# Optimization experiments

Hardware: AMD Instinct MI355X
Metric: run time of the kernel (lower is better)

The kernel has to match this reference:

```python
import jax, jax.numpy as jnp
import numpy as np

N_NODES = 100000
N_EDGES = 1600000
IN_FEATS = 128
HIDDEN = 128
NUM_CLASSES = 64


def setup_inputs() -> dict:
    key = jax.random.key(0)
    k1, k2, k3, k4, k5 = jax.random.split(key, 5)
    inputs = jax.random.normal(k1, (N_NODES, IN_FEATS), dtype=jnp.float32)
    src = jax.random.randint(k2, (N_EDGES,), 0, N_NODES, dtype=jnp.int32)
    dst = jax.random.randint(k3, (N_EDGES,), 0, N_NODES, dtype=jnp.int32)
    W1 = jax.random.normal(k4, (IN_FEATS, HIDDEN), dtype=jnp.float32) / np.sqrt(IN_FEATS)
    b1 = jnp.zeros((HIDDEN,), dtype=jnp.float32)
    W2 = jax.random.normal(k5, (HIDDEN, NUM_CLASSES), dtype=jnp.float32) / np.sqrt(HIDDEN)
    b2 = jnp.zeros((NUM_CLASSES,), dtype=jnp.float32)
    return {"inputs": inputs, "src": src, "dst": dst, "W1": W1, "b1": b1, "W2": W2, "b2": b2}


def _graph_conv(x, src, dst, W, b, n_nodes):
    # DGL GraphConv, norm='both': h = D_in^{-1/2} A D_out^{-1/2} x W + b
    ones = jnp.ones(src.shape[0], dtype=x.dtype)
    deg_out = jax.ops.segment_sum(ones, src, num_segments=n_nodes)
    deg_in = jax.ops.segment_sum(ones, dst, num_segments=n_nodes)
    norm_src = jax.lax.rsqrt(jnp.clip(deg_out, 1.0))  # [N]
    norm_dst = jax.lax.rsqrt(jnp.clip(deg_in, 1.0))   # [N]
    x = x * norm_src[:, None]
    msgs = x[src]                                      # [E, d] gather
    agg = jax.ops.segment_sum(msgs, dst, num_segments=n_nodes)  # [N, d] scatter-add
    agg = agg * norm_dst[:, None]
    return agg @ W + b


def reference(inputs, src, dst, W1, b1, W2, b2):
    n = inputs.shape[0]
    h = _graph_conv(inputs, src, dst, W1, b1, n)
    h = jax.nn.relu(h)
    h = _graph_conv(h, src, dst, W2, b2, n)
    return h
```

## Files before the change

kernel.cpp:

```cpp
#include <hip/hip_runtime.h>
#include <hip/hip_bf16.h>

#define N_FEATS_IN 128
#define BK_BITS 8
#define BK_SIZE 256
#define EPB 4096
#define MAXNB 512

typedef _Float16 h8 __attribute__((ext_vector_type(8)));
typedef float    f4v __attribute__((ext_vector_type(4)));
typedef float    f8v __attribute__((ext_vector_type(8)));

__device__ inline int wave_incl_scan(int v) {
    const int lane = threadIdx.x & 63;
    for (int off = 1; off < 64; off <<= 1) {
        int u = __shfl_up(v, off, 64);
        if (lane >= off) v += u;
    }
    return v;
}

__device__ inline int block_excl_scan(int s, int* ws, int* total) {
    const int lane = threadIdx.x & 63, wid = threadIdx.x >> 6;
    int inc = wave_incl_scan(s);
    if (lane == 63) ws[wid] = inc;
    __syncthreads();
    int woff = 0;
#pragma unroll
    for (int w = 0; w < 4; ++w) woff += (w < wid) ? ws[w] : 0;
    if (total) *total = ws[0] + ws[1] + ws[2] + ws[3];
    return woff + inc - s;
}

__global__ __launch_bounds__(256) void hist_kernel(
    const int* __restrict__ src, const int* __restrict__ dst,
    int* __restrict__ bh_d, int* __restrict__ bh_s, int E, int NB) {
    __shared__ int hd[MAXNB];
    __shared__ int hs[MAXNB];
    const int t = threadIdx.x;
    for (int i = t; i < NB; i += 256) { hd[i] = 0; hs[i] = 0; }
    __syncthreads();
    const int base = blockIdx.x * EPB;
    const int end = min(base + EPB, E);
    for (int e = base + t; e < end; e += 256) {
        atomicAdd(&hd[dst[e] >> BK_BITS], 1);
        atomicAdd(&hs[src[e] >> BK_BITS], 1);
    }
    __syncthreads();
    for (int i = t; i < NB; i += 256) {
        bh_d[(size_t)blockIdx.x * NB + i] = hd[i];
        bh_s[(size_t)blockIdx.x * NB + i] = hs[i];
    }
}

__global__ __launch_bounds__(256) void colsum2_kernel(
    const int* __restrict__ bh_d, const int* __restrict__ bh_s,
    int* __restrict__ tot_d, int* __restrict__ tot_s, int NBLK, int NB) {
    __shared__ int ws[8];
    const int b = blockIdx.x;
    const int t = threadIdx.x;
    const int lane = t & 63, wid = t >> 6;
    int sd = 0, ss = 0;
    for (int r = t; r < NBLK; r += 256) {
        sd += bh_d[(size_t)r * NB + b];
        ss += bh_s[(size_t)r * NB + b];
    }
    for (int off = 1; off < 64; off <<= 1) {
        sd += __shfl_down(sd, off, 64);
        ss += __shfl_down(ss, off, 64);
    }
    if (lane == 0) { ws[wid] = sd; ws[4 + wid] = ss; }
    __syncthreads();
    if (t == 0) tot_d[b] = ws[0] + ws[1] + ws[2] + ws[3];
    if (t == 1) tot_s[b] = ws[4] + ws[5] + ws[6] + ws[7];
}

__global__ __launch_bounds__(256) void bscan2_kernel(
    const int* __restrict__ tot_d, const int* __restrict__ tot_s,
    int* __restrict__ gb_d, int* __restrict__ gb_s,
    int* __restrict__ row_ptr, int NB, int N, int E) {
    __shared__ int ws[4];
    const int t = threadIdx.x;
    {
        const int a = (2 * t < NB) ? tot_d[2 * t] : 0;
        const int b = (2 * t + 1 < NB) ? tot_d[2 * t + 1] : 0;
        const int excl = block_excl_scan(a + b, ws, nullptr);
        if (2 * t < NB) gb_d[2 * t] = excl;
        if (2 * t + 1 < NB) gb_d[2 * t + 1] = excl + a;
    }
    __syncthreads();
    {
        const int a = (2 * t < NB) ? tot_s[2 * t] : 0;
        const int b = (2 * t + 1 < NB) ? tot_s[2 * t + 1] : 0;
        const int excl = block_excl_scan(a + b, ws, nullptr);
        if (2 * t < NB) gb_s[2 * t] = excl;
        if (2 * t + 1 < NB) gb_s[2 * t + 1] = excl + a;
    }
    if (t == 0) { gb_d[NB] = E; gb_s[NB] = E; row_ptr[N] = E; }
}

__global__ __launch_bounds__(256) void colscan2_kernel(
    int* __restrict__ bh_d, int* __restrict__ bh_s,
    const int* __restrict__ gb_d, const int* __restrict__ gb_s,
    int NBLK, int NB) {
    __shared__ int ws[4];
    const int b = blockIdx.x;
    const int t = threadIdx.x;
    const int r0 = 2 * t, r1 = 2 * t + 1;
    {
        const int a = (r0 < NBLK) ? bh_d[(size_t)r0 * NB + b] : 0;
        const int c = (r1 < NBLK) ? bh_d[(size_t)r1 * NB + b] : 0;
        const int excl = block_excl_scan(a + c, ws, nullptr);
        const int base = gb_d[b];
        if (r0 < NBLK) bh_d[(size_t)r0 * NB + b] = base + excl;
        if (r1 < NBLK) bh_d[(size_t)r1 * NB + b] = base + excl + a;
    }
    __syncthreads();
    {
        const int a = (r0 < NBLK) ? bh_s[(size_t)r0 * NB + b] : 0;
        const int c = (r1 < NBLK) ? bh_s[(size_t)r1 * NB + b] : 0;
        const int excl = block_excl_scan(a + c, ws, nullptr);
        const int base = gb_s[b];
        if (r0 < NBLK) bh_s[(size_t)r0 * NB + b] = base + excl;
        if (r1 < NBLK) bh_s[(size_t)r1 * NB + b] = base + excl + a;
    }
}

__global__ __launch_bounds__(256) void scatter2_kernel(
    const int* __restrict__ src, const int* __restrict__ dst,
    const int* __restrict__ bh_d, const int* __restrict__ bh_s,
    unsigned int* __restrict__ ebuf, unsigned char* __restrict__ sbuf,
    int E, int NB) {
    __shared__ int cd[MAXNB];
    __shared__ int cs[MAXNB];
    const int t = threadIdx.x;
    for (int i = t; i < NB; i += 256) {
        cd[i] = bh_d[(size_t)blockIdx.x * NB + i];
        cs[i] = bh_s[(size_t)blockIdx.x * NB + i];
    }
    __syncthreads();
    const int base = blockIdx.x * EPB;
    const int end = min(base + EPB, E);
    for (int e = base + t; e < end; e += 256) {
        const int d = dst[e];
        const int s = src[e];
        const int pd = atomicAdd(&cd[d >> BK_BITS], 1);
        ebuf[pd] = ((unsigned)s << 8) | (unsigned)(d & (BK_SIZE - 1));
        const int ps = atomicAdd(&cs[s >> BK_BITS], 1);
        sbuf[ps] = (unsigned char)(s & (BK_SIZE - 1));
    }
}

__global__ __launch_bounds__(256) void bucket_csr_kernel(
    const unsigned int* __restrict__ ebuf, const int* __restrict__ gb_d,
    int* __restrict__ row_ptr, float* __restrict__ norm_dst,
    int* __restrict__ edge_src, int N) {
    __shared__ int cnt[BK_SIZE];
    __shared__ int lro[BK_SIZE];
    __shared__ int ws[4];
    const int b = blockIdx.x;
    const int t = threadIdx.x;
    const int beg = gb_d[b], end = gb_d[b + 1];

    cnt[t] = 0;
    __syncthreads();
    for (int j = beg + t; j < end; j += 256)
        atomicAdd(&cnt[ebuf[j] & (BK_SIZE - 1)], 1);
    __syncthreads();

    const int v = cnt[t];
    const int excl = block_excl_scan(v, ws, nullptr);
    lro[t] = beg + excl;
    const int node = b * BK_SIZE + t;
    if (node < N) {
        row_ptr[node] = beg + excl;
        norm_dst[node] = rsqrtf(fmaxf((float)v, 1.0f));
    }
    __syncthreads();
    cnt[t] = 0;
    __syncthreads();

    for (int j = beg + t; j < end; j += 256) {
        const unsigned int ed = ebuf[j];
        const int dl = ed & (BK_SIZE - 1);
        const int p = atomicAdd(&cnt[dl], 1);
        edge_src[lro[dl] + p] = (int)(ed >> 8);
    }
}

__global__ __launch_bounds__(256) void count_src_kernel(
    const unsigned char* __restrict__ sbuf, const int* __restrict__ gb_s,
    float* __restrict__ norm_src, int N) {
    __shared__ int cnt[BK_SIZE];
    const int b = blockIdx.x;
    const int t = threadIdx.x;
    const int beg = gb_s[b], end = gb_s[b + 1];
    cnt[t] = 0;
    __syncthreads();
    for (int j = beg + t; j < end; j += 256)
        atomicAdd(&cnt[sbuf[j]], 1);
    __syncthreads();
    const int node = b * BK_SIZE + t;
    if (node < N)
        norm_src[node] = rsqrtf(fmaxf((float)cnt[t], 1.0f));
}

template <int OC, bool XHALF>
__global__ __launch_bounds__(256) void mfma_gemm_kernel(
    const void* __restrict__ Xv, const float* __restrict__ W,
    const float* __restrict__ scale, _Float16* __restrict__ Y, int n) {
    constexpr int K = 128;
    constexpr int NT = OC / 16;
    constexpr int RPB = 128;
    __shared__ _Float16 Wf[NT * 4 * 64 * 8];

    const int tid = threadIdx.x;
    for (int i = tid; i < K * OC; i += 256) {
        const int k = i / OC, c = i % OC;
        const int t = c >> 4, s = k >> 5, q = (k >> 3) & 3, j = k & 7;
        Wf[(((t * 4 + s) * 4 + q) * 16 + (c & 15)) * 8 + j] = (_Float16)W[i];
    }
    __syncthreads();

    const int lane = tid & 63;
    const int wv = tid >> 6;
    const int m = lane & 15, q = lane >> 4;

#pragma unroll
    for (int it = 0; it < RPB / 64; ++it) {
        const int rbase = blockIdx.x * RPB + it * 64 + wv * 16;
        const int lrow = min(rbase + m, n - 1);

        h8 a[4];
        if constexpr (XHALF) {
            const _Float16* X = (const _Float16*)Xv;
            const _Float16* p = &X[(size_t)lrow * K + q * 8];
#pragma unroll
            for (int s = 0; s < 4; ++s) a[s] = *(const h8*)(p + s * 32);
        } else {
            const float* X = (const float*)Xv;
            const float* p = &X[(size_t)lrow * K + q * 8];
#pragma unroll
            for (int s = 0; s < 4; ++s) {
                const float4 u0 = *(const float4*)(p + s * 32);
                const float4 u1 = *(const float4*)(p + s * 32 + 4);
                h8 v;
                v[0] = (_Float16)u0.x; v[1] = (_Float16)u0.y;
                v[2] = (_Float16)u0.z; v[3] = (_Float16)u0.w;
                v[4] = (_Float16)u1.x; v[5] = (_Float16)u1.y;
                v[6] = (_Float16)u1.z; v[7] = (_Float16)u1.w;
                a[s] = v;
            }
        }

        f4v acc[NT];
#pragma unroll
        for (int t = 0; t < NT; ++t) acc[t] = (f4v)0.0f;

#pragma unroll
        for (int s = 0; s < 4; ++s) {
#pragma unroll
            for (int t = 0; t < NT; ++t) {
                const h8 b = *(const h8*)&Wf[((t * 4 + s) * 64 + lane) * 8];
                acc[t] = __builtin_amdgcn_mfma_f32_16x16x32_f16(
                    a[s], b, acc[t], 0, 0, 0);
            }
        }

#pragma unroll
        for (int r = 0; r < 4; ++r) {
            const int orow = rbase + q * 4 + r;
            if (orow < n) {
                const float sc = scale[orow];
#pragma unroll
                for (int t = 0; t < NT; ++t)
                    Y[(size_t)orow * OC + t * 16 + m] =
                        (_Float16)(acc[t][r] * sc);
            }
        }
    }
}

template <int FEAT, bool RELU, bool OUT_HALF>
__global__ __launch_bounds__(256) void gather_agg_kernel(
    const _Float16* __restrict__ T, const int* __restrict__ row_ptr,
    const int* __restrict__ edge_src, const float* __restrict__ norm_dst,
    const float* __restrict__ bias, void* __restrict__ outv, int n) {
    constexpr int TPN = FEAT / 8;
    constexpr int NPB = 256 / TPN;
    const int node = blockIdx.x * NPB + threadIdx.x / TPN;
    const int f8 = threadIdx.x % TPN;
    if (node >= n) return;
    const int beg = row_ptr[node];
    const int end = row_ptr[node + 1];
    const h8* T8 = (const h8*)T;

    f8v acc = (f8v)0.0f;
    int j = beg;
    for (; j + 7 < end; j += 8) {
        int s[8];
#pragma unroll
        for (int u = 0; u < 8; ++u) s[u] = edge_src[j + u];
        h8 a[8];
#pragma unroll
        for (int u = 0; u < 8; ++u) a[u] = T8[(size_t)s[u] * TPN + f8];
#pragma unroll
        for (int u = 0; u < 8; ++u)
            acc += __builtin_convertvector(a[u], f8v);
    }
    for (; j + 3 < end; j += 4) {
        int s[4];
#pragma unroll
        for (int u = 0; u < 4; ++u) s[u] = edge_src[j + u];
        h8 a[4];
#pragma unroll
        for (int u = 0; u < 4; ++u) a[u] = T8[(size_t)s[u] * TPN + f8];
#pragma unroll
        for (int u = 0; u < 4; ++u)
            acc += __builtin_convertvector(a[u], f8v);
    }
    for (; j < end; ++j)
        acc += __builtin_convertvector(T8[(size_t)edge_src[j] * TPN + f8], f8v);

    const float nd = norm_dst[node];
    float r[8];
#pragma unroll
    for (int k = 0; k < 8; ++k) {
        r[k] = acc[k] * nd + bias[f8 * 8 + k];
        if constexpr (RELU) r[k] = fmaxf(r[k], 0.0f);
    }

    if constexpr (OUT_HALF) {
        _Float16* out = (_Float16*)outv;
        h8 o;
#pragma unroll
        for (int k = 0; k < 8; ++k) o[k] = (_Float16)r[k];
        *(h8*)&out[(size_t)node * FEAT + f8 * 8] = o;
    } else {
        float* out = (float*)outv;
        float4 o0 = make_float4(r[0], r[1], r[2], r[3]);
        float4 o1 = make_float4(r[4], r[5], r[6], r[7]);
        *(float4*)&out[(size_t)node * FEAT + f8 * 8] = o0;
        *(float4*)&out[(size_t)node * FEAT + f8 * 8 + 4] = o1;
    }
}

extern "C" void kernel_launch(void* const* d_in, const int* in_sizes, int n_in,
                              void* d_out, int out_size, void* d_ws, size_t ws_size,
                              hipStream_t stream) {
    const float* x   = (const float*)d_in[0];
    const int*   src = (const int*)d_in[1];
    const int*   dst = (const int*)d_in[2];
    const float* W1  = (const float*)d_in[3];
    const float* b1  = (const float*)d_in[4];
    const float* W2  = (const float*)d_in[5];
    const float* b2  = (const float*)d_in[6];
    float* out = (float*)d_out;

    const int N = in_sizes[0] / N_FEATS_IN;
    const int E = in_sizes[1];
    const int NB = (N + BK_SIZE - 1) / BK_SIZE;
    const int NBLK = (E + EPB - 1) / EPB;

    auto align4 = [](size_t w) { return (w + 3) & ~(size_t)3; };
    char* base = (char*)d_ws;
    size_t off = 0;
    auto take = [&](size_t words) {
        char* p = base + off * 4;
        off = align4(off + words);
        return p;
    };
    int*   tot_d    = (int*)take(NB);
    int*   tot_s    = (int*)take(NB);
    int*   gb_d     = (int*)take(NB + 1);
    int*   gb_s     = (int*)take(NB + 1);
    int*   bh_d     = (int*)take((size_t)NBLK * NB);
    int*   bh_s     = (int*)take((size_t)NBLK * NB);
    unsigned int*  ebuf = (unsigned int*)take(E);
    unsigned char* sbuf = (unsigned char*)take((E + 3) / 4);
    int*   row_ptr  = (int*)take(N + 1);
    int*   edge_src = (int*)take(E);
    float* norms    = (float*)take(2 * (size_t)N);
    _Float16* t1    = (_Float16*)take((size_t)N * 64);
    _Float16* h1    = (_Float16*)take((size_t)N * 64);
    _Float16* t2    = (_Float16*)take((size_t)N * 32);
    float* norm_src = norms;
    float* norm_dst = norms + N;

    hist_kernel<<<NBLK, 256, 0, stream>>>(src, dst, bh_d, bh_s, E, NB);
    colsum2_kernel<<<NB, 256, 0, stream>>>(bh_d, bh_s, tot_d, tot_s, NBLK, NB);
    bscan2_kernel<<<1, 256, 0, stream>>>(tot_d, tot_s, gb_d, gb_s, row_ptr,
                                         NB, N, E);
    colscan2_kernel<<<NB, 256, 0, stream>>>(bh_d, bh_s, gb_d, gb_s, NBLK, NB);
    scatter2_kernel<<<NBLK, 256, 0, stream>>>(src, dst, bh_d, bh_s, ebuf, sbuf,
                                              E, NB);
    bucket_csr_kernel<<<NB, 256, 0, stream>>>(ebuf, gb_d, row_ptr, norm_dst,
                                              edge_src, N);
    count_src_kernel<<<NB, 256, 0, stream>>>(sbuf, gb_s, norm_src, N);

    mfma_gemm_kernel<128, false><<<(N + 127) / 128, 256, 0, stream>>>(
        x, W1, norm_src, t1, N);
    gather_agg_kernel<128, true, true><<<(N + 15) / 16, 256, 0, stream>>>(
        t1, row_ptr, edge_src, norm_dst, b1, h1, N);

    mfma_gemm_kernel<64, true><<<(N + 127) / 128, 256, 0, stream>>>(
        h1, W2, norm_src, t2, N);
    gather_agg_kernel<64, false, false><<<(N + 31) / 32, 256, 0, stream>>>(
        t2, row_ptr, edge_src, norm_dst, b2, out, N);
}
```

Baseline: 343.1 us.

## Split gather-aggregate over feature chunks and use nontemporal index loads

Rewrites the neighbor gather-aggregate so each block handles only one of eight feature slices for a larger group of nodes, aiming to shrink the working set of gathered rows per pass for better cache reuse. Index and row-pointer reads plus output stores become nontemporal, and the 8-edge unrolled loop is removed. The trade-off is that the CSR indices are re-read once per chunk and each per-row access becomes narrower, which may hurt coalescing.

```diff
diff --git a/kernel.cpp b/kernel.cpp
--- a/kernel.cpp
+++ b/kernel.cpp
@@ -282,51 +282,49 @@
 }
 
 template <int FEAT, bool RELU, bool OUT_HALF>
-__global__ __launch_bounds__(256) void gather_agg_kernel(
+__global__ __launch_bounds__(256) void gather_chunk_kernel(
     const _Float16* __restrict__ T, const int* __restrict__ row_ptr,
     const int* __restrict__ edge_src, const float* __restrict__ norm_dst,
     const float* __restrict__ bias, void* __restrict__ outv, int n) {
-    constexpr int TPN = FEAT / 8;
+    constexpr int CF = FEAT / 8;
+    constexpr int TPN = CF / 8;
     constexpr int NPB = 256 / TPN;
-    const int node = blockIdx.x * NPB + threadIdx.x / TPN;
+    constexpr int VS = FEAT / 8;
+
+    const int chunk = blockIdx.x & 7;
+    const int grp = blockIdx.x >> 3;
+    const int node = grp * NPB + threadIdx.x / TPN;
     const int f8 = threadIdx.x % TPN;
     if (node >= n) return;
-    const int beg = row_ptr[node];
-    const int end = row_ptr[node + 1];
+    const int beg = __builtin_nontemporal_load(&row_ptr[node]);
+    const int end = __builtin_nontemporal_load(&row_ptr[node + 1]);
     const h8* T8 = (const h8*)T;
+    const int voff = chunk * TPN + f8;
 
     f8v acc = (f8v)0.0f;
     int j = beg;
-    for (; j + 7 < end; j += 8) {
-        int s[8];
-#pragma unroll
-        for (int u = 0; u < 8; ++u) s[u] = edge_src[j + u];
-        h8 a[8];
-#pragma unroll
-        for (int u = 0; u < 8; ++u) a[u] = T8[(size_t)s[u] * TPN + f8];
-#pragma unroll
-        for (int u = 0; u < 8; ++u)
-            acc += __builtin_convertvector(a[u], f8v);
-    }
     for (; j + 3 < end; j += 4) {
         int s[4];
 #pragma unroll
-        for (int u = 0; u < 4; ++u) s[u] = edge_src[j + u];
+        for (int u = 0; u < 4; ++u)
+            s[u] = __builtin_nontemporal_load(&edge_src[j + u]);
         h8 a[4];
 #pragma unroll
-        for (int u = 0; u < 4; ++u) a[u] = T8[(size_t)s[u] * TPN + f8];
+        for (int u = 0; u < 4; ++u) a[u] = T8[(size_t)s[u] * VS + voff];
 #pragma unroll
         for (int u = 0; u < 4; ++u)
             acc += __builtin_convertvector(a[u], f8v);
     }
-    for (; j < end; ++j)
-        acc += __builtin_convertvector(T8[(size_t)edge_src[j] * TPN + f8], f8v);
+    for (; j < end; ++j) {
+        const int s = __builtin_nontemporal_load(&edge_src[j]);
+        acc += __builtin_convertvector(T8[(size_t)s * VS + voff], f8v);
+    }
 
     const float nd = norm_dst[node];
     float r[8];
 #pragma unroll
     for (int k = 0; k < 8; ++k) {
-        r[k] = acc[k] * nd + bias[f8 * 8 + k];
+        r[k] = acc[k] * nd + bias[chunk * CF + f8 * 8 + k];
         if constexpr (RELU) r[k] = fmaxf(r[k], 0.0f);
     }
 
@@ -335,13 +333,15 @@
         h8 o;
 #pragma unroll
         for (int k = 0; k < 8; ++k) o[k] = (_Float16)r[k];
-        *(h8*)&out[(size_t)node * FEAT + f8 * 8] = o;
+        __builtin_nontemporal_store(
+            o, (h8*)&out[(size_t)node * FEAT + chunk * CF + f8 * 8]);
     } else {
         float* out = (float*)outv;
-        float4 o0 = make_float4(r[0], r[1], r[2], r[3]);
-        float4 o1 = make_float4(r[4], r[5], r[6], r[7]);
-        *(float4*)&out[(size_t)node * FEAT + f8 * 8] = o0;
-        *(float4*)&out[(size_t)node * FEAT + f8 * 8 + 4] = o1;
+        f4v o0 = {r[0], r[1], r[2], r[3]};
+        f4v o1 = {r[4], r[5], r[6], r[7]};
+        float* p = &out[(size_t)node * FEAT + chunk * CF + f8 * 8];
+        __builtin_nontemporal_store(o0, (f4v*)p);
+        __builtin_nontemporal_store(o1, (f4v*)(p + 4));
     }
 }
 
@@ -400,11 +400,13 @@
 
     mfma_gemm_kernel<128, false><<<(N + 127) / 128, 256, 0, stream>>>(
         x, W1, norm_src, t1, N);
-    gather_agg_kernel<128, true, true><<<(N + 15) / 16, 256, 0, stream>>>(
+    gather_chunk_kernel<128, true, true>
+        <<<8 * ((N + 127) / 128), 256, 0, stream>>>(
         t1, row_ptr, edge_src, norm_dst, b1, h1, N);
 
     mfma_gemm_kernel<64, true><<<(N + 127) / 128, 256, 0, stream>>>(
         h1, W2, norm_src, t2, N);
-    gather_agg_kernel<64, false, false><<<(N + 31) / 32, 256, 0, stream>>>(
+    gather_chunk_kernel<64, false, false>
+        <<<8 * ((N + 255) / 256), 256, 0, stream>>>(
         t2, row_ptr, edge_src, norm_dst, b2, out, N);
 }
```

Result: slower. 778.3 us (+126.8%).

## Merge column sum and column scan, fold source-degree count into CSR kernel

Applied to the files above, without the earlier changes.

Replaces the separate column-sum and column-scan passes over the per-block histograms with a single kernel that computes local column prefixes and totals in one pass. The global bucket offsets are now added while the scatter kernel loads its counters. The source-degree counting kernel is folded into the bucket CSR kernel. Together this removes two kernel launches and one read/write pass over the histogram arrays, in exchange for a slightly longer serial tail in the fused CSR kernel.

```diff
diff --git a/kernel.cpp b/kernel.cpp
--- a/kernel.cpp
+++ b/kernel.cpp
@@ -53,26 +53,34 @@
     }
 }
 
-__global__ __launch_bounds__(256) void colsum2_kernel(
-    const int* __restrict__ bh_d, const int* __restrict__ bh_s,
+__global__ __launch_bounds__(256) void colprefix2_kernel(
+    int* __restrict__ bh_d, int* __restrict__ bh_s,
     int* __restrict__ tot_d, int* __restrict__ tot_s, int NBLK, int NB) {
-    __shared__ int ws[8];
+    __shared__ int ws[4];
     const int b = blockIdx.x;
     const int t = threadIdx.x;
-    const int lane = t & 63, wid = t >> 6;
-    int sd = 0, ss = 0;
-    for (int r = t; r < NBLK; r += 256) {
-        sd += bh_d[(size_t)r * NB + b];
-        ss += bh_s[(size_t)r * NB + b];
-    }
-    for (int off = 1; off < 64; off <<= 1) {
-        sd += __shfl_down(sd, off, 64);
-        ss += __shfl_down(ss, off, 64);
-    }
-    if (lane == 0) { ws[wid] = sd; ws[4 + wid] = ss; }
-    __syncthreads();
-    if (t == 0) tot_d[b] = ws[0] + ws[1] + ws[2] + ws[3];
-    if (t == 1) tot_s[b] = ws[4] + ws[5] + ws[6] + ws[7];
+    int carry = 0;
+    for (int base = 0; base < NBLK; base += 256) {
+        const int r = base + t;
+        const int v = (r < NBLK) ? bh_d[(size_t)r * NB + b] : 0;
+        int total;
+        const int e = block_excl_scan(v, ws, &total);
+        if (r < NBLK) bh_d[(size_t)r * NB + b] = carry + e;
+        carry += total;
+        __syncthreads();
+    }
+    if (t == 0) tot_d[b] = carry;
+    carry = 0;
+    for (int base = 0; base < NBLK; base += 256) {
+        const int r = base + t;
+        const int v = (r < NBLK) ? bh_s[(size_t)r * NB + b] : 0;
+        int total;
+        const int e = block_excl_scan(v, ws, &total);
+        if (r < NBLK) bh_s[(size_t)r * NB + b] = carry + e;
+        carry += total;
+        __syncthreads();
+    }
+    if (t == 0) tot_s[b] = carry;
 }
 
 __global__ __launch_bounds__(256) void bscan2_kernel(
@@ -99,44 +107,18 @@
     if (t == 0) { gb_d[NB] = E; gb_s[NB] = E; row_ptr[N] = E; }
 }
 
-__global__ __launch_bounds__(256) void colscan2_kernel(
-    int* __restrict__ bh_d, int* __restrict__ bh_s,
-    const int* __restrict__ gb_d, const int* __restrict__ gb_s,
-    int NBLK, int NB) {
-    __shared__ int ws[4];
-    const int b = blockIdx.x;
-    const int t = threadIdx.x;
-    const int r0 = 2 * t, r1 = 2 * t + 1;
-    {
-        const int a = (r0 < NBLK) ? bh_d[(size_t)r0 * NB + b] : 0;
-        const int c = (r1 < NBLK) ? bh_d[(size_t)r1 * NB + b] : 0;
-        const int excl = block_excl_scan(a + c, ws, nullptr);
-        const int base = gb_d[b];
-        if (r0 < NBLK) bh_d[(size_t)r0 * NB + b] = base + excl;
-        if (r1 < NBLK) bh_d[(size_t)r1 * NB + b] = base + excl + a;
-    }
-    __syncthreads();
-    {
-        const int a = (r0 < NBLK) ? bh_s[(size_t)r0 * NB + b] : 0;
-        const int c = (r1 < NBLK) ? bh_s[(size_t)r1 * NB + b] : 0;
-        const int excl = block_excl_scan(a + c, ws, nullptr);
-        const int base = gb_s[b];
-        if (r0 < NBLK) bh_s[(size_t)r0 * NB + b] = base + excl;
-        if (r1 < NBLK) bh_s[(size_t)r1 * NB + b] = base + excl + a;
-    }
-}
-
 __global__ __launch_bounds__(256) void scatter2_kernel(
     const int* __restrict__ src, const int* __restrict__ dst,
     const int* __restrict__ bh_d, const int* __restrict__ bh_s,
+    const int* __restrict__ gb_d, const int* __restrict__ gb_s,
     unsigned int* __restrict__ ebuf, unsigned char* __restrict__ sbuf,
     int E, int NB) {
     __shared__ int cd[MAXNB];
     __shared__ int cs[MAXNB];
     const int t = threadIdx.x;
     for (int i = t; i < NB; i += 256) {
-        cd[i] = bh_d[(size_t)blockIdx.x * NB + i];
-        cs[i] = bh_s[(size_t)blockIdx.x * NB + i];
+        cd[i] = bh_d[(size_t)blockIdx.x * NB + i] + gb_d[i];
+        cs[i] = bh_s[(size_t)blockIdx.x * NB + i] + gb_s[i];
     }
     __syncthreads();
     const int base = blockIdx.x * EPB;
@@ -153,14 +135,16 @@
 
 __global__ __launch_bounds__(256) void bucket_csr_kernel(
     const unsigned int* __restrict__ ebuf, const int* __restrict__ gb_d,
+    const unsigned char* __restrict__ sbuf, const int* __restrict__ gb_s,
     int* __restrict__ row_ptr, float* __restrict__ norm_dst,
-    int* __restrict__ edge_src, int N) {
+    float* __restrict__ norm_src, int* __restrict__ edge_src, int N) {
     __shared__ int cnt[BK_SIZE];
     __shared__ int lro[BK_SIZE];
     __shared__ int ws[4];
     const int b = blockIdx.x;
     const int t = threadIdx.x;
     const int beg = gb_d[b], end = gb_d[b + 1];
+    const int node = b * BK_SIZE + t;
 
     cnt[t] = 0;
     __syncthreads();
@@ -171,7 +155,6 @@
     const int v = cnt[t];
     const int excl = block_excl_scan(v, ws, nullptr);
     lro[t] = beg + excl;
-    const int node = b * BK_SIZE + t;
     if (node < N) {
         row_ptr[node] = beg + excl;
         norm_dst[node] = rsqrtf(fmaxf((float)v, 1.0f));
@@ -186,21 +169,14 @@
         const int p = atomicAdd(&cnt[dl], 1);
         edge_src[lro[dl] + p] = (int)(ed >> 8);
     }
-}
-
-__global__ __launch_bounds__(256) void count_src_kernel(
-    const unsigned char* __restrict__ sbuf, const int* __restrict__ gb_s,
-    float* __restrict__ norm_src, int N) {
-    __shared__ int cnt[BK_SIZE];
-    const int b = blockIdx.x;
-    const int t = threadIdx.x;
-    const int beg = gb_s[b], end = gb_s[b + 1];
+
+    __syncthreads();
     cnt[t] = 0;
     __syncthreads();
-    for (int j = beg + t; j < end; j += 256)
+    const int sb = gb_s[b], se = gb_s[b + 1];
+    for (int j = sb + t; j < se; j += 256)
         atomicAdd(&cnt[sbuf[j]], 1);
     __syncthreads();
-    const int node = b * BK_SIZE + t;
     if (node < N)
         norm_src[node] = rsqrtf(fmaxf((float)cnt[t], 1.0f));
 }
@@ -388,15 +364,14 @@
     float* norm_dst = norms + N;
 
     hist_kernel<<<NBLK, 256, 0, stream>>>(src, dst, bh_d, bh_s, E, NB);
-    colsum2_kernel<<<NB, 256, 0, stream>>>(bh_d, bh_s, tot_d, tot_s, NBLK, NB);
+    colprefix2_kernel<<<NB, 256, 0, stream>>>(bh_d, bh_s, tot_d, tot_s,
+                                              NBLK, NB);
     bscan2_kernel<<<1, 256, 0, stream>>>(tot_d, tot_s, gb_d, gb_s, row_ptr,
                                          NB, N, E);
-    colscan2_kernel<<<NB, 256, 0, stream>>>(bh_d, bh_s, gb_d, gb_s, NBLK, NB);
-    scatter2_kernel<<<NBLK, 256, 0, stream>>>(src, dst, bh_d, bh_s, ebuf, sbuf,
-                                              E, NB);
-    bucket_csr_kernel<<<NB, 256, 0, stream>>>(ebuf, gb_d, row_ptr, norm_dst,
-                                              edge_src, N);
-    count_src_kernel<<<NB, 256, 0, stream>>>(sbuf, gb_s, norm_src, N);
+    scatter2_kernel<<<NBLK, 256, 0, stream>>>(src, dst, bh_d, bh_s, gb_d, gb_s,
+                                              ebuf, sbuf, E, NB);
+    bucket_csr_kernel<<<NB, 256, 0, stream>>>(ebuf, gb_d, sbuf, gb_s, row_ptr,
+                                              norm_dst, norm_src, edge_src, N);
 
     mfma_gemm_kernel<128, false><<<(N + 127) / 128, 256, 0, stream>>>(
         x, W1, norm_src, t1, N);
```

Result: faster. 336.4 us (-2.0%).
